# Performance work log

Measured on AMD Instinct MI355X. Metric: run time of the kernel, lower is better.

## Reference

```python
import jax, jax.numpy as jnp
import numpy as np
from jax import lax

CONV1_T = 15.0
CONV2_T = 10.0
K2 = 8
R2 = 1


def _conv2d(x, w):
    # F.conv2d, stride 1, no padding, no bias
    return lax.conv_general_dilated(x, w, (1, 1), 'VALID',
                                    dimension_numbers=('NCHW', 'OIHW', 'NCHW'))


def _pad(x, p):
    return jnp.pad(x, ((0, 0), (0, 0), (p, p), (p, p)))


def _fire(pot, thr):
    # sf.fire: threshold_(pot, thr, 0) (strictly greater), spikes = sign
    pot_t = jnp.where(pot > thr, pot, jnp.zeros((), pot.dtype))
    return jnp.sign(pot_t), pot_t


def _max_pool(x, k, s):
    return lax.reduce_window(x, jnp.array(-jnp.inf, x.dtype), lax.max,
                             (1, 1, k, k), (1, 1, s, s), 'VALID')


def _pointwise_inhibition(pot):
    # sf.pointwise_inhibition: keep, at each (h,w), only the feature that spikes
    # earliest (ties broken by max potential); zero it entirely if nothing fired.
    T, C, H, W = pot.shape
    max_vals = pot.max(axis=1)                      # [T,H,W]
    max_idx = pot.argmax(axis=1)                    # [T,H,W] winning feature per t
    clamp = jnp.sign(max_vals)                      # [T,H,W] did any feature spike at t
    earliest = jnp.clip((T - clamp.sum(axis=0)).astype(jnp.int32), 0, T - 1)  # [H,W]
    win_feat = jnp.take_along_axis(max_idx, earliest[None].astype(max_idx.dtype), axis=0)[0]  # [H,W]
    fired_last = clamp[-1]                          # [H,W] any spike by final step
    rows = jnp.arange(H)[:, None]
    cols = jnp.arange(W)[None, :]
    coef = jnp.zeros((C, H, W), pot.dtype).at[win_feat, rows, cols].set(fired_last)
    return pot * coef[None]


def _get_k_winners(pot, spk, kwta, r):
    # sf.get_k_winners: rank neurons by (earliness, potential), iterative argmax
    # with per-feature and spatial-radius inhibition (NMS-like).
    T, C, H, W = pot.shape
    earliest = jnp.clip((T - spk.sum(axis=0)).astype(jnp.int32), 0, T - 1)  # [C,H,W]
    values = jnp.take_along_axis(pot, earliest[None], axis=0)[0]            # [C,H,W]
    trunc = spk * values[None]
    v = trunc.max() * T
    trunc = trunc + spk * v
    total = trunc.sum(axis=0)                                               # [C,H,W]

    def step(tot, _):
        flat = tot.reshape(-1)
        idx = jnp.argmax(flat).astype(jnp.int32)
        mval = flat[idx]
        c = idx // (H * W)
        rem = idx % (H * W)
        row = rem // W
        col = rem % W
        fmask = (jnp.arange(C) == c)[:, None, None]
        rmask = (jnp.abs(jnp.arange(H) - row) <= r)[None, :, None]
        cmask = (jnp.abs(jnp.arange(W) - col) <= r)[None, None, :]
        tot = jnp.where(fmask | (rmask & cmask), jnp.zeros((), tot.dtype), tot)
        winner = jnp.where(mval > 0, jnp.stack([c, row, col]),
                           jnp.full((3,), -1, jnp.int32))
        return tot, winner

    _, winners = lax.scan(step, total, None, length=kwta)
    return winners  # [kwta, 3] = (feature, row, col), -1 padded


def setup_inputs():
    key = jax.random.key(0)
    k1, k2, k3 = jax.random.split(key, 3)
    # cumulative spike-wave input [T=15, C=6, H=252, W=252]
    inp = jax.random.randint(k1, (15, 6, 252, 252), 0, 2, dtype=jnp.int32)
    # snn.Convolution weights ~ N(mean=0.8, std=0.05)
    w1 = 0.8 + 0.05 * jax.random.normal(k2, (30, 6, 5, 5), dtype=jnp.float32)
    w2 = 0.8 + 0.05 * jax.random.normal(k3, (250, 30, 3, 3), dtype=jnp.float32)
    return {"input": inp, "max_layer": 2, "w1": w1, "w2": w2}


def reference(input, max_layer, w1, w2):
    # training path, max_layer == 2
    x = _pad(input.astype(jnp.float32), 2)        # [15,6,256,256]
    pot = _conv2d(x, w1)                          # [15,30,252,252]
    spk, pot = _fire(pot, CONV1_T)
    spk_in = _pad(_max_pool(spk, 2, 2), 1)        # [15,30,128,128]
    pot = _conv2d(spk_in, w2)                     # [15,250,126,126]
    spk, pot = _fire(pot, CONV2_T)
    pot = _pointwise_inhibition(pot)
    spk = jnp.sign(pot)
    winners = _get_k_winners(pot, spk, K2, R2)
    return spk, pot, winners
```

## Files before the change

### kernel.cpp

```cpp
#include <hip/hip_runtime.h>
#include <limits.h>

#define T_STEPS 15
#define CIN     6
#define HIN     252
#define C1      30
#define SH      128
#define SW      128
#define C2      250
#define NPIX    15876
#define NTP     (T_STEPS*NPIX)
#define THR1    15.0f
#define THR2    10.0f
#define KWTA    8
#define SPK_ELEMS  59535000L

__global__ __launch_bounds__(256) void consts_k(
    const float* __restrict__ w2, float* __restrict__ wT,
    float* __restrict__ Sthr, float* __restrict__ consts) {
  const int f = threadIdx.x;
  if (blockIdx.x < 270) {
    int k = blockIdx.x;
    wT[k * 256 + f] = (f < C2) ? w2[(long)f * 270 + k] : 0.f;
    return;
  }
  __shared__ float sS[256];
  float S = 0.f;
  if (f < C2) {
    const float* wf = w2 + (long)f * 270;
    for (int k = 0; k < 270; ++k) S = fmaf(wf[k], 1.0f, S);
  }
  float st = (f < C2 && S > THR2) ? S : 0.f;
  Sthr[f] = st;
  sS[f] = (f < C2) ? st : -1.f;
  __syncthreads();
  if (f == 0) {
    float bv = -1.f; int bf = 0;
    for (int i = 0; i < C2; ++i) { if (sS[i] > bv) { bv = sS[i]; bf = i; } }
    consts[0] = bv;
    ((int*)consts)[1] = bf;
  }
}

#define G1 5
__global__ __launch_bounds__(128, 6) void conv1_v4(
    const int* __restrict__ inp, const float* __restrict__ w1,
    float* __restrict__ spk_in) {
  __shared__ float srow[6][256];
  const int ph = blockIdx.x;
  const int cg = blockIdx.y;
  const int t  = blockIdx.z;
  const int pw = threadIdx.x;

  float acc[G1][4];
  #pragma unroll
  for (int cc = 0; cc < G1; ++cc) {
    acc[cc][0] = 0.f; acc[cc][1] = 0.f; acc[cc][2] = 0.f; acc[cc][3] = 0.f;
  }

  for (int ic = 0; ic < CIN; ++ic) {
    __syncthreads();
    for (int i = pw; i < 6 * 256; i += 128) {
      int rr = i >> 8, col = i & 255;
      int row = 2 * ph - 2 + rr, in_col = col - 2;
      float v = 0.f;
      if (row >= 0 && row < HIN && in_col >= 0 && in_col < HIN)
        v = (float)inp[((long)(t * CIN + ic) * HIN + row) * HIN + in_col];
      srow[rr][col] = v;
    }
    __syncthreads();

    #pragma unroll
    for (int rr = 0; rr < 6; ++rr) {
      float row6[6];
      #pragma unroll
      for (int j = 0; j < 6; ++j)
        row6[j] = srow[rr][(2 * pw + j) & 255];
      #pragma unroll
      for (int cc = 0; cc < G1; ++cc) {
        const int c = cg * G1 + cc;
        const float* wp = w1 + ((c * CIN) + ic) * 25;
        if (rr < 5) {
          #pragma unroll
          for (int kw = 0; kw < 5; ++kw) {
            float wv = wp[rr * 5 + kw];
            acc[cc][0] = fmaf(wv, row6[kw],     acc[cc][0]);
            acc[cc][1] = fmaf(wv, row6[kw + 1], acc[cc][1]);
          }
        }
        if (rr >= 1) {
          #pragma unroll
          for (int kw = 0; kw < 5; ++kw) {
            float wv = wp[(rr - 1) * 5 + kw];
            acc[cc][2] = fmaf(wv, row6[kw],     acc[cc][2]);
            acc[cc][3] = fmaf(wv, row6[kw + 1], acc[cc][3]);
          }
        }
      }
    }
  }
  if (pw < 126) {
    #pragma unroll
    for (int cc = 0; cc < G1; ++cc) {
      int c = cg * G1 + cc;
      bool fired = acc[cc][0] > THR1 || acc[cc][1] > THR1 ||
                   acc[cc][2] > THR1 || acc[cc][3] > THR1;
      spk_in[((long)(t * C1 + c) * SH + (ph + 1)) * SW + (pw + 1)] = fired ? 1.f : 0.f;
    }
  }
}

__global__ __launch_bounds__(128) void classify(
    const float* __restrict__ spk_in, const float* __restrict__ consts,
    float* __restrict__ meta_val, int* __restrict__ meta_f,
    unsigned char* __restrict__ allones) {
  const int oh = blockIdx.x, t = blockIdx.y, ow = threadIdx.x;
  if (ow >= 126) return;
  const float* base = spk_in + (long)t * C1 * SH * SW;
  float prod = 1.f;
  for (int c = 0; c < C1; ++c) {
    const float* bp = base + (c * SH + oh) * SW + ow;
    #pragma unroll
    for (int kh = 0; kh < 3; ++kh)
      prod *= bp[kh * SW] * bp[kh * SW + 1] * bp[kh * SW + 2];
  }
  int tp = t * NPIX + oh * 126 + ow;
  bool ao = prod > 0.5f;
  allones[tp] = ao ? 1 : 0;
  if (ao) { meta_val[tp] = consts[0]; meta_f[tp] = ((const int*)consts)[1]; }
}

__global__ __launch_bounds__(256) void dense_meta(
    const float* __restrict__ spk_in, const float* __restrict__ wT,
    const unsigned char* __restrict__ allones,
    float* __restrict__ meta_val, int* __restrict__ meta_f) {
  __shared__ int s_list[256];
  __shared__ int s_cnt;
  __shared__ float s_win[270][8];
  __shared__ unsigned long long s_part[4];
  const int tid = threadIdx.x;
  if (tid == 0) s_cnt = 0;
  __syncthreads();
  {
    int i = blockIdx.x + tid * 1024;
    if (i < NTP && !allones[i]) { int pos = atomicAdd(&s_cnt, 1); s_list[pos] = i; }
  }
  __syncthreads();
  const int cnt = s_cnt;
  for (int g = 0; g < cnt; g += 8) {
    int m = cnt - g; if (m > 8) m = 8;
    for (int j = tid; j < 270 * 8; j += 256) {
      int k = j >> 3, q = j & 7;
      float v = 0.f;
      if (q < m) {
        int tp = s_list[g + q];
        int t = tp / NPIX, p = tp % NPIX;
        int oh = p / 126, ow = p % 126;
        int c = k / 9, kh = (k % 9) / 3, kw = k % 3;
        v = spk_in[((long)(t * C1 + c) * SH + oh + kh) * SW + ow + kw];
      }
      s_win[k][q] = v;
    }
    __syncthreads();
    float acc[8];
    #pragma unroll
    for (int q = 0; q < 8; ++q) acc[q] = 0.f;
    for (int k = 0; k < 270; ++k) {
      float wv = wT[k * 256 + tid];
      #pragma unroll
      for (int q = 0; q < 8; ++q)
        acc[q] = fmaf(wv, s_win[k][q], acc[q]);
    }
    #pragma unroll
    for (int q = 0; q < 8; ++q) {
      unsigned long long key = 0;
      if (tid < C2) {
        float v = acc[q] > THR2 ? acc[q] : 0.f;
        key = ((unsigned long long)__float_as_uint(v) << 8) | (unsigned)(255 - tid);
      }
      #pragma unroll
      for (int s = 1; s < 64; s <<= 1) {
        unsigned long long o = __shfl_xor(key, s, 64);
        if (o > key) key = o;
      }
      if ((tid & 63) == 0) s_part[tid >> 6] = key;
      __syncthreads();
      if (tid == 0 && q < m) {
        unsigned long long k0 = s_part[0];
        if (s_part[1] > k0) k0 = s_part[1];
        if (s_part[2] > k0) k0 = s_part[2];
        if (s_part[3] > k0) k0 = s_part[3];
        int tp = s_list[g + q];
        meta_val[tp] = __uint_as_float((unsigned)(k0 >> 8));
        meta_f[tp] = 255 - (int)(k0 & 255);
      }
      __syncthreads();
    }
  }
}

__global__ __launch_bounds__(256) void inhibit2(
    const float* __restrict__ meta_val, const int* __restrict__ meta_f,
    int* __restrict__ winfeat) {
  int p = blockIdx.x * 256 + threadIdx.x;
  if (p >= NPIX) return;
  int n = 0; bool last = false;
  #pragma unroll
  for (int t = 0; t < T_STEPS; ++t) {
    bool fr = meta_val[t * NPIX + p] > 0.f;
    n += fr ? 1 : 0;
    if (t == T_STEPS - 1) last = fr;
  }
  int e = T_STEPS - n;
  if (e > T_STEPS - 1) e = T_STEPS - 1;
  if (e < 0) e = 0;
  winfeat[p] = last ? meta_f[e * NPIX + p] : -1;
}

__global__ __launch_bounds__(256) void winner_pv(
    const int* __restrict__ winfeat, const unsigned char* __restrict__ allones,
    const float* __restrict__ Sthr, const float* __restrict__ spk_in,
    const float* __restrict__ w2, float* __restrict__ spk_out,
    float* __restrict__ pot_out, float* __restrict__ pvbuf) {
  int tp = blockIdx.x * 256 + threadIdx.x;
  if (tp >= NTP) return;
  int t = tp / NPIX, p = tp % NPIX;
  int w = winfeat[p];
  if (w < 0) { pvbuf[tp] = 0.f; return; }
  float pt;
  if (allones[tp]) {
    pt = Sthr[w];
  } else {
    int oh = p / 126, ow = p % 126;
    const float* wb = w2 + (long)w * 270;
    float a = 0.f;
    for (int c = 0; c < C1; ++c) {
      const float* sb = spk_in + ((long)(t * C1 + c) * SH + oh) * SW + ow;
      #pragma unroll
      for (int kh = 0; kh < 3; ++kh)
        #pragma unroll
        for (int kw = 0; kw < 3; ++kw)
          a = fmaf(wb[c * 9 + kh * 3 + kw], sb[kh * SW + kw], a);
    }
    pt = a > THR2 ? a : 0.f;
  }
  pvbuf[tp] = pt;
  long o = ((long)t * C2 + w) * NPIX + p;
  pot_out[o] = pt;
  spk_out[o] = pt > 0.f ? 1.f : 0.f;
}

__global__ __launch_bounds__(256) void cand_k(
    const int* __restrict__ winfeat, const float* __restrict__ pvbuf,
    float* __restrict__ cand_val, int* __restrict__ cand_n) {
  int p = blockIdx.x * 256 + threadIdx.x;
  if (p >= NPIX) return;
  int w = winfeat[p];
  if (w < 0) { cand_val[p] = 0.f; cand_n[p] = 0; return; }
  float pv[T_STEPS]; int n = 0;
  #pragma unroll
  for (int t = 0; t < T_STEPS; ++t) {
    float v = pvbuf[t * NPIX + p];
    pv[t] = v;
    n += v > 0.f ? 1 : 0;
  }
  int e = T_STEPS - n; if (e > 14) e = 14; if (e < 0) e = 0;
  float cv = 0.f;
  #pragma unroll
  for (int t = 0; t < T_STEPS; ++t) if (t == e) cv = pv[t];
  cand_val[p] = cv;
  cand_n[p] = n;
}

__global__ __launch_bounds__(1024) void kwin_select(
    const float* __restrict__ cand_val, const int* __restrict__ cand_n,
    const int* __restrict__ winfeat, float* __restrict__ winners_out) {
  __shared__ float r_val[1024];
  __shared__ int   r_idx[1024];
  __shared__ unsigned char featrem[C2];
  __shared__ unsigned char rem[NPIX];
  __shared__ int s_rw, s_cw;
  const int tid = threadIdx.x;

  for (int i = tid; i < C2; i += 1024) featrem[i] = 0;
  for (int i = tid; i < NPIX; i += 1024) rem[i] = 0;

  float m = 0.f;
  for (int i = tid; i < NPIX; i += 1024) m = fmaxf(m, cand_val[i]);
  r_val[tid] = m;
  __syncthreads();
  for (int s = 512; s > 0; s >>= 1) {
    if (tid < s) r_val[tid] = fmaxf(r_val[tid], r_val[tid + s]);
    __syncthreads();
  }
  const float v = r_val[0] * (float)T_STEPS;
  __syncthreads();

  for (int round = 0; round < KWTA; ++round) {
    float bv = 0.f; int bi = INT_MAX;
    for (int p = tid; p < NPIX; p += 1024) {
      if (rem[p]) continue;
      int w = winfeat[p];
      if (w < 0 || featrem[w]) continue;
      float x = cand_val[p] + v;
      int n = cand_n[p];
      float tot = 0.f;
      for (int q = 0; q < n; ++q) tot += x;
      int flat = w * NPIX + p;
      if (tot > bv || (tot == bv && flat < bi)) { bv = tot; bi = flat; }
    }
    r_val[tid] = bv; r_idx[tid] = bi;
    __syncthreads();
    for (int s = 512; s > 0; s >>= 1) {
      if (tid < s) {
        float ov = r_val[tid + s]; int oi = r_idx[tid + s];
        if (ov > r_val[tid] || (ov == r_val[tid] && oi < r_idx[tid])) {
          r_val[tid] = ov; r_idx[tid] = oi;
        }
      }
      __syncthreads();
    }
    if (tid == 0) {
      float mv = r_val[0]; int fi = r_idx[0];
      if (mv > 0.f && fi != INT_MAX) {
        int c = fi / NPIX; int p = fi % NPIX;
        int row = p / 126, col = p % 126;
        winners_out[round * 3 + 0] = (float)c;
        winners_out[round * 3 + 1] = (float)row;
        winners_out[round * 3 + 2] = (float)col;
        featrem[c] = 1;
        s_rw = row; s_cw = col;
      } else {
        winners_out[round * 3 + 0] = -1.f;
        winners_out[round * 3 + 1] = -1.f;
        winners_out[round * 3 + 2] = -1.f;
        s_rw = -10; s_cw = -10;
      }
    }
    __syncthreads();
    int rw = s_rw, cw = s_cw;
    if (rw >= 0) {
      for (int p = tid; p < NPIX; p += 1024) {
        int row = p / 126, col = p % 126;
        if (row >= rw - 1 && row <= rw + 1 && col >= cw - 1 && col <= cw + 1)
          rem[p] = 1;
      }
    }
    __syncthreads();
  }
}

extern "C" void kernel_launch(void* const* d_in, const int* in_sizes, int n_in,
                              void* d_out, int out_size, void* d_ws, size_t ws_size,
                              hipStream_t stream) {
  const int*   inp = (const int*)d_in[0];
  const float* w1  = (const float*)d_in[2];
  const float* w2  = (const float*)d_in[3];

  float* out = (float*)d_out;
  float* spk_out = out;
  float* pot_out = out + SPK_ELEMS;
  float* win_out = out + 2 * SPK_ELEMS;

  float* ws = (float*)d_ws;
  float* spk_in   = ws;
  float* meta_val = ws + 7372800;
  int*   meta_f   = (int*)ws + 7610940;
  int*   winfeat  = (int*)ws + 7849080;
  float* cand_val = ws + 7864956;
  int*   cand_n   = (int*)ws + 7880832;
  float* Sthr     = ws + 7896708;
  float* consts   = ws + 7896964;
  float* wT       = ws + 7896968;
  unsigned char* allones = (unsigned char*)(ws + 7966088);

  hipMemsetAsync(spk_in, 0, 7372800 * sizeof(float), stream);
  hipMemsetAsync(out, 0, 2 * SPK_ELEMS * sizeof(float), stream);

  consts_k<<<271, 256, 0, stream>>>(w2, wT, Sthr, consts);
  {
    dim3 g(126, 6, 15);
    conv1_v4<<<g, 128, 0, stream>>>(inp, w1, spk_in);
  }
  {
    dim3 g(126, 15);
    classify<<<g, 128, 0, stream>>>(spk_in, consts, meta_val, meta_f, allones);
  }
  dense_meta<<<1024, 256, 0, stream>>>(spk_in, wT, allones, meta_val, meta_f);
  inhibit2<<<(NPIX + 255) / 256, 256, 0, stream>>>(meta_val, meta_f, winfeat);
  winner_pv<<<(NTP + 255) / 256, 256, 0, stream>>>(
      winfeat, allones, Sthr, spk_in, w2, spk_out, pot_out, meta_val );
  cand_k<<<(NPIX + 255) / 256, 256, 0, stream>>>(winfeat, meta_val, cand_val, cand_n);
  kwin_select<<<1, 1024, 0, stream>>>(cand_val, cand_n, winfeat, win_out);
}
```

Before: 811.0 us.

## Pack conv1 spikes into bitmasks for classify and speed up k-winner selection

conv1 now also emits a per-row bitmask of fired pixels via wave ballots. classify reads those 64-bit words and checks all-ones 3x3 windows with bitwise ANDs and shifts, replacing 270 float loads and multiplies per pixel. kwin_select caches totals and feature ids in LDS once and packs value and index into a single 64-bit key, so each round uses shuffle reductions instead of a shared-memory tree with many syncs. This adds a small extra memset and bitmap write, and depends on the key packing preserving the original tie-break order.

```diff
diff --git a/kernel.cpp b/kernel.cpp
--- a/kernel.cpp
+++ b/kernel.cpp
@@ -43,10 +43,11 @@
 }
 
 #define G1 5
-__global__ __launch_bounds__(128, 6) void conv1_v4(
+__global__ __launch_bounds__(128, 6) void conv1_v4b(
     const int* __restrict__ inp, const float* __restrict__ w1,
-    float* __restrict__ spk_in) {
+    float* __restrict__ spk_in, unsigned long long* __restrict__ bitm) {
   __shared__ float srow[6][256];
+  __shared__ unsigned long long s_bal[2][G1];
   const int ph = blockIdx.x;
   const int cg = blockIdx.y;
   const int t  = blockIdx.z;
@@ -99,33 +100,50 @@
       }
     }
   }
-  if (pw < 126) {
-    #pragma unroll
-    for (int cc = 0; cc < G1; ++cc) {
+  unsigned fbits = 0;
+  #pragma unroll
+  for (int cc = 0; cc < G1; ++cc) {
+    bool fired = (pw < 126) && (acc[cc][0] > THR1 || acc[cc][1] > THR1 ||
+                                acc[cc][2] > THR1 || acc[cc][3] > THR1);
+    if (fired) fbits |= 1u << cc;
+    if (pw < 126) {
       int c = cg * G1 + cc;
-      bool fired = acc[cc][0] > THR1 || acc[cc][1] > THR1 ||
-                   acc[cc][2] > THR1 || acc[cc][3] > THR1;
       spk_in[((long)(t * C1 + c) * SH + (ph + 1)) * SW + (pw + 1)] = fired ? 1.f : 0.f;
     }
   }
-}
-
-__global__ __launch_bounds__(128) void classify(
-    const float* __restrict__ spk_in, const float* __restrict__ consts,
+  #pragma unroll
+  for (int cc = 0; cc < G1; ++cc) {
+    unsigned long long b = __ballot((fbits >> cc) & 1);
+    if ((pw & 63) == 0) s_bal[pw >> 6][cc] = b;
+  }
+  __syncthreads();
+  if (pw < G1) {
+    unsigned long long b0 = s_bal[0][pw], b1 = s_bal[1][pw];
+    unsigned long long w0 = b0 << 1;
+    unsigned long long w1 = (b1 << 1) | (b0 >> 63);
+    int c = cg * G1 + pw;
+    unsigned long long* bp = bitm + 2 * (((long)(t * C1 + c)) * SH + (ph + 1));
+    bp[0] = w0; bp[1] = w1;
+  }
+}
+
+__global__ __launch_bounds__(128) void classify2(
+    const unsigned long long* __restrict__ bitm, const float* __restrict__ consts,
     float* __restrict__ meta_val, int* __restrict__ meta_f,
     unsigned char* __restrict__ allones) {
   const int oh = blockIdx.x, t = blockIdx.y, ow = threadIdx.x;
+  unsigned long long lo = ~0ull, hi = ~0ull;
+  for (int c = 0; c < C1; ++c) {
+    const unsigned long long* bp = bitm + 2 * (((long)(t * C1 + c)) * SH + oh);
+    lo &= bp[0] & bp[2] & bp[4];
+    hi &= bp[1] & bp[3] & bp[5];
+  }
   if (ow >= 126) return;
-  const float* base = spk_in + (long)t * C1 * SH * SW;
-  float prod = 1.f;
-  for (int c = 0; c < C1; ++c) {
-    const float* bp = base + (c * SH + oh) * SW + ow;
-    #pragma unroll
-    for (int kh = 0; kh < 3; ++kh)
-      prod *= bp[kh * SW] * bp[kh * SW + 1] * bp[kh * SW + 2];
-  }
+  unsigned long long x = (ow < 64)
+      ? ((lo >> ow) | (ow ? (hi << (64 - ow)) : 0ull))
+      : (hi >> (ow - 64));
+  bool ao = (x & 7ull) == 7ull;
   int tp = t * NPIX + oh * 126 + ow;
-  bool ao = prod > 0.5f;
   allones[tp] = ao ? 1 : 0;
   if (ao) { meta_val[tp] = consts[0]; meta_f[tp] = ((const int*)consts)[1]; }
 }
@@ -272,78 +290,94 @@
   cand_n[p] = n;
 }
 
-__global__ __launch_bounds__(1024) void kwin_select(
+__global__ __launch_bounds__(1024) void kwin_select2(
     const float* __restrict__ cand_val, const int* __restrict__ cand_n,
     const int* __restrict__ winfeat, float* __restrict__ winners_out) {
-  __shared__ float r_val[1024];
-  __shared__ int   r_idx[1024];
-  __shared__ unsigned char featrem[C2];
-  __shared__ unsigned char rem[NPIX];
-  __shared__ int s_rw, s_cw;
+  __shared__ float s_tot[NPIX];
+  __shared__ unsigned char s_w[NPIX];
+  __shared__ unsigned char s_rem[NPIX];
+  __shared__ unsigned char s_fr[256];
+  __shared__ unsigned long long s_part[16];
+  __shared__ float s_max[16];
+  __shared__ int s_sel;
   const int tid = threadIdx.x;
-
-  for (int i = tid; i < C2; i += 1024) featrem[i] = 0;
-  for (int i = tid; i < NPIX; i += 1024) rem[i] = 0;
+  const int wid = tid >> 6, lane = tid & 63;
+
+  if (tid < 256) s_fr[tid] = 0;
 
   float m = 0.f;
-  for (int i = tid; i < NPIX; i += 1024) m = fmaxf(m, cand_val[i]);
-  r_val[tid] = m;
-  __syncthreads();
-  for (int s = 512; s > 0; s >>= 1) {
-    if (tid < s) r_val[tid] = fmaxf(r_val[tid], r_val[tid + s]);
-    __syncthreads();
-  }
-  const float v = r_val[0] * (float)T_STEPS;
+  for (int p = tid; p < NPIX; p += 1024) {
+    int w = winfeat[p];
+    s_w[p] = (w < 0) ? 255 : (unsigned char)w;
+    s_rem[p] = 0;
+    float cv = cand_val[p];
+    s_tot[p] = cv;
+    m = fmaxf(m, cv);
+  }
+  #pragma unroll
+  for (int s = 1; s < 64; s <<= 1) m = fmaxf(m, __shfl_xor(m, s, 64));
+  if (lane == 0) s_max[wid] = m;
+  __syncthreads();
+  if (tid == 0) {
+    float mm = s_max[0];
+    for (int i = 1; i < 16; ++i) mm = fmaxf(mm, s_max[i]);
+    s_max[0] = mm * (float)T_STEPS;
+  }
+  __syncthreads();
+  const float v = s_max[0];
+  for (int p = tid; p < NPIX; p += 1024) {
+    float x = s_tot[p] + v;
+    int n = cand_n[p];
+    float tot = 0.f;
+    for (int q = 0; q < n; ++q) tot += x;
+    s_tot[p] = tot;
+  }
   __syncthreads();
 
   for (int round = 0; round < KWTA; ++round) {
-    float bv = 0.f; int bi = INT_MAX;
+    unsigned long long best = 0;
     for (int p = tid; p < NPIX; p += 1024) {
-      if (rem[p]) continue;
-      int w = winfeat[p];
-      if (w < 0 || featrem[w]) continue;
-      float x = cand_val[p] + v;
-      int n = cand_n[p];
-      float tot = 0.f;
-      for (int q = 0; q < n; ++q) tot += x;
-      int flat = w * NPIX + p;
-      if (tot > bv || (tot == bv && flat < bi)) { bv = tot; bi = flat; }
-    }
-    r_val[tid] = bv; r_idx[tid] = bi;
-    __syncthreads();
-    for (int s = 512; s > 0; s >>= 1) {
-      if (tid < s) {
-        float ov = r_val[tid + s]; int oi = r_idx[tid + s];
-        if (ov > r_val[tid] || (ov == r_val[tid] && oi < r_idx[tid])) {
-          r_val[tid] = ov; r_idx[tid] = oi;
-        }
-      }
-      __syncthreads();
-    }
+      unsigned char w = s_w[p];
+      if (w == 255 || s_rem[p] || s_fr[w]) continue;
+      unsigned long long flat = (unsigned long long)w * NPIX + (unsigned)p;
+      unsigned long long key =
+          ((unsigned long long)__float_as_uint(s_tot[p]) << 25) | (0x1FFFFFFull - flat);
+      if (key > best) best = key;
+    }
+    #pragma unroll
+    for (int s = 1; s < 64; s <<= 1) {
+      unsigned long long o = __shfl_xor(best, s, 64);
+      if (o > best) best = o;
+    }
+    if (lane == 0) s_part[wid] = best;
+    __syncthreads();
     if (tid == 0) {
-      float mv = r_val[0]; int fi = r_idx[0];
-      if (mv > 0.f && fi != INT_MAX) {
-        int c = fi / NPIX; int p = fi % NPIX;
-        int row = p / 126, col = p % 126;
+      unsigned long long b = s_part[0];
+      for (int i = 1; i < 16; ++i) if (s_part[i] > b) b = s_part[i];
+      float tot = __uint_as_float((unsigned)(b >> 25));
+      if (b != 0 && tot > 0.f) {
+        int flat = (int)(0x1FFFFFFull - (b & 0x1FFFFFFull));
+        int c = flat / NPIX, p = flat % NPIX;
         winners_out[round * 3 + 0] = (float)c;
-        winners_out[round * 3 + 1] = (float)row;
-        winners_out[round * 3 + 2] = (float)col;
-        featrem[c] = 1;
-        s_rw = row; s_cw = col;
+        winners_out[round * 3 + 1] = (float)(p / 126);
+        winners_out[round * 3 + 2] = (float)(p % 126);
+        s_fr[c] = 1;
+        s_sel = p;
       } else {
         winners_out[round * 3 + 0] = -1.f;
         winners_out[round * 3 + 1] = -1.f;
         winners_out[round * 3 + 2] = -1.f;
-        s_rw = -10; s_cw = -10;
-      }
-    }
-    __syncthreads();
-    int rw = s_rw, cw = s_cw;
-    if (rw >= 0) {
+        s_sel = -1;
+      }
+    }
+    __syncthreads();
+    int sel = s_sel;
+    if (sel >= 0) {
+      int rw = sel / 126, cw = sel % 126;
       for (int p = tid; p < NPIX; p += 1024) {
         int row = p / 126, col = p % 126;
         if (row >= rw - 1 && row <= rw + 1 && col >= cw - 1 && col <= cw + 1)
-          rem[p] = 1;
+          s_rem[p] = 1;
       }
     }
     __syncthreads();
@@ -373,23 +407,25 @@
   float* consts   = ws + 7896964;
   float* wT       = ws + 7896968;
   unsigned char* allones = (unsigned char*)(ws + 7966088);
+  unsigned long long* bitm = (unsigned long long*)(ws + 8025624);
 
   hipMemsetAsync(spk_in, 0, 7372800 * sizeof(float), stream);
+  hipMemsetAsync(bitm, 0, 115200 * sizeof(unsigned long long), stream);
   hipMemsetAsync(out, 0, 2 * SPK_ELEMS * sizeof(float), stream);
 
   consts_k<<<271, 256, 0, stream>>>(w2, wT, Sthr, consts);
   {
     dim3 g(126, 6, 15);
-    conv1_v4<<<g, 128, 0, stream>>>(inp, w1, spk_in);
+    conv1_v4b<<<g, 128, 0, stream>>>(inp, w1, spk_in, bitm);
   }
   {
     dim3 g(126, 15);
-    classify<<<g, 128, 0, stream>>>(spk_in, consts, meta_val, meta_f, allones);
+    classify2<<<g, 128, 0, stream>>>(bitm, consts, meta_val, meta_f, allones);
   }
   dense_meta<<<1024, 256, 0, stream>>>(spk_in, wT, allones, meta_val, meta_f);
   inhibit2<<<(NPIX + 255) / 256, 256, 0, stream>>>(meta_val, meta_f, winfeat);
   winner_pv<<<(NTP + 255) / 256, 256, 0, stream>>>(
       winfeat, allones, Sthr, spk_in, w2, spk_out, pot_out, meta_val );
   cand_k<<<(NPIX + 255) / 256, 256, 0, stream>>>(winfeat, meta_val, cand_val, cand_n);
-  kwin_select<<<1, 1024, 0, stream>>>(cand_val, cand_n, winfeat, win_out);
-}
+  kwin_select2<<<1, 1024, 0, stream>>>(cand_val, cand_n, winfeat, win_out);
+}
```

New measurement: 795.6 us. No clear change (-1.9%).
